# Kernel tuning notes

Hardware: AMD Instinct MI355X
Metric: run time of the kernel (lower is better)

The kernel has to match this reference:

```python
import jax, jax.numpy as jnp
import numpy as np

B, NR, NF, NH, NFH, D, HID = 32, 32, 128, 64, 64, 32, 256


def setup_inputs() -> dict:
    key = jax.random.key(0)
    ks = jax.random.split(key, 16)

    def w(k, o, i):
        return (jax.random.normal(k, (o, i), jnp.float32) / np.sqrt(i)).astype(jnp.float32)

    inp = {
        "robot": jax.random.normal(ks[0], (B, NR, D), jnp.float32),
        "frontier": jax.random.normal(ks[1], (B, NF, D), jnp.float32),
        "robot_history": jax.random.normal(ks[2], (B, NH, D), jnp.float32),
        "frontier_history": jax.random.normal(ks[3], (B, NFH, D), jnp.float32),
        "robot_frontier": jax.random.uniform(ks[4], (B, NR, NF), jnp.float32),
        "robot_past": jax.random.uniform(ks[5], (B, NR, NH), jnp.float32),
        "frontier_past": jax.random.uniform(ks[6], (B, NF, NFH), jnp.float32),
        # parameters (torch Linear convention: weight [out, in])
        "Wq": w(ks[7], D, D), "bq": jnp.zeros(D, jnp.float32),
        "Wk": w(ks[8], D, D), "bk": jnp.zeros(D, jnp.float32),
        "Wv": w(ks[9], D, D), "bv": jnp.zeros(D, jnp.float32),
        "Wn1": w(ks[10], HID, 2 * D), "bn1": jnp.zeros(HID, jnp.float32),
        "Wn2": w(ks[11], D, HID), "bn2": jnp.zeros(D, jnp.float32),
        "We1": w(ks[12], HID, 2 * D + 1), "be1": jnp.zeros(HID, jnp.float32),
        "We2": w(ks[13], 1, HID), "be2": jnp.zeros(1, jnp.float32),
    }
    return inp


def reference(robot, frontier, robot_history, frontier_history, robot_frontier,
              robot_past, frontier_past, Wq, bq, Wk, bk, Wv, bv,
              Wn1, bn1, Wn2, bn2, We1, be1, We2, be2):
    def lin(x, W, b):
        return x @ W.T + b

    def nmlp(h):
        return lin(jax.nn.relu(lin(h, Wn1, bn1)), Wn2, bn2)

    def emlp(h):
        return lin(jax.nn.relu(lin(h, We1, be1)), We2, be2)

    def intra(x):  # x: [b, n, D]
        q, k, v = lin(x, Wq, bq), lin(x, Wk, bk), lin(x, Wv, bv)
        e = jax.nn.softmax(jnp.einsum('bnd,bmd->bnm', q, k), axis=-1)
        agg = jnp.einsum('bnm,bmd->bnd', e, v)
        return x + nmlp(jnp.concatenate([x, agg], axis=-1))

    def inter(x, y, dis):  # x: [b,Nx,D], y: [b,Ny,D], dis: [b,Nx,Ny]
        xq, yk, yv = lin(x, Wq, bq), lin(y, Wk, bk), lin(y, Wv, bv)
        b, Nx, _ = x.shape
        Ny = y.shape[1]
        r_i = jnp.broadcast_to(xq[:, :, None, :], (b, Nx, Ny, D))
        f_j = jnp.broadcast_to(yk[:, None, :, :], (b, Nx, Ny, D))
        edge_input = jnp.concatenate([r_i, f_j, dis[..., None]], axis=-1)  # [b,Nx,Ny,65]
        score = emlp(edge_input)[..., 0]                                   # [b,Nx,Ny]
        e = jax.nn.softmax(score, axis=-1)
        agg = jnp.einsum('bnm,bmd->bnd', e, yv)
        x = x + nmlp(jnp.concatenate([x, agg], axis=-1))
        return e, x

    robot = intra(robot)
    frontier = intra(frontier)           # == per-sample intra on [1,Nf,D]
    robot_history = intra(robot_history)
    frontier_history = intra(frontier_history)
    _, robot = inter(robot, robot_history, robot_past)
    _, new_frontier = inter(frontier, frontier_history, frontier_past)
    edge, robot = inter(robot, new_frontier, robot_frontier)
    # original returns the intra-transformed frontier (split_frontier), not new_frontier
    return (robot, frontier, robot_history, frontier_history, edge)
```

## Files before the change

### kernel.cpp

```cpp
#include <hip/hip_runtime.h>

#define BATCH 32
#define NRr 32
#define NFf 128
#define NHh 64
#define NFHh 64
#define TI 4

__device__ __forceinline__ float dot4(float4 a, float4 b) {
    return fmaf(a.x, b.x, fmaf(a.y, b.y, fmaf(a.z, b.z, a.w * b.w)));
}

__global__ __launch_bounds__(256) void intra_kernel(
    const float* __restrict__ robot, const float* __restrict__ frontier,
    const float* __restrict__ rhist, const float* __restrict__ fhist,
    const float* __restrict__ Wq, const float* __restrict__ bq,
    const float* __restrict__ Wk, const float* __restrict__ bk,
    const float* __restrict__ Wv, const float* __restrict__ bv,
    const float* __restrict__ Wn1, const float* __restrict__ bn1,
    const float* __restrict__ Wn2, const float* __restrict__ bn2,
    float* __restrict__ o_robot, float* __restrict__ o_frontier,
    float* __restrict__ o_rh, float* __restrict__ o_fh)
{
    __shared__ __align__(16) float sXc[1024];
    __shared__ __align__(16) float sQ[1024];
    __shared__ __align__(16) float sQK[1024];
    __shared__ __align__(16) float sAgg[1024];
    __shared__ __align__(16) float sBig[8448];
    float* sS  = sBig;
    float* sXT = sBig + 4224;
    float* sT  = sBig;

    const int blk = blockIdx.x, tid = threadIdx.x;
    const float* xin; float* xout; int N, lgN, b, chunk;
    if (blk < 32)       { xin=robot;    xout=o_robot;    N=32;  lgN=5; b=blk;          chunk=0; }
    else if (blk < 160) { xin=frontier; xout=o_frontier; N=128; lgN=7; b=(blk-32)>>2;  chunk=(blk-32)&3; }
    else if (blk < 224) { xin=rhist;    xout=o_rh;       N=64;  lgN=6; b=(blk-160)>>1; chunk=(blk-160)&1; }
    else                { xin=fhist;    xout=o_fh;       N=64;  lgN=6; b=(blk-224)>>1; chunk=(blk-224)&1; }

    const int P = N + 4, P2 = N + 1;
    const float* xb = xin + (size_t)b * N * 32;
    const int r0 = chunk << 5;
    const int d = tid & 31;

    {
        int idx = tid;
        #pragma unroll
        for (int it = 0; it < 4; ++it, idx += 256)
            sXc[idx] = xb[(r0 << 5) + idx];
    }
    for (int idx = tid; idx < (N << 5); idx += 256) {
        int j = idx >> 5, d2 = idx & 31;
        sXT[d2 * P2 + j] = xb[idx];
    }
    __syncthreads();

    {
        const float4* wq4 = (const float4*)(Wq + (d << 5));
        float4 wq[8];
        #pragma unroll
        for (int k = 0; k < 8; ++k) wq[k] = wq4[k];
        const float bqd = bq[d];
        int idx = tid;
        #pragma unroll
        for (int it = 0; it < 4; ++it, idx += 256) {
            int r = idx >> 5;
            const float4* xr = (const float4*)(sXc + (r << 5));
            float a = bqd;
            #pragma unroll
            for (int k = 0; k < 8; ++k) a += dot4(wq[k], xr[k]);
            sQ[idx] = a;
        }
    }
    __syncthreads();

    {
        int idx = tid;
        #pragma unroll
        for (int it = 0; it < 4; ++it, idx += 256) {
            int r = idx >> 5, e = idx & 31;
            const float* qr = sQ + (r << 5);
            float a = 0.f;
            #pragma unroll
            for (int dd2 = 0; dd2 < 32; ++dd2)
                a = fmaf(Wk[dd2 * 32 + e], qr[dd2], a);
            sQK[idx] = a;
        }
    }
    __syncthreads();

    for (int idx = tid; idx < (N << 5); idx += 256) {
        int r = idx >> lgN, j = idx & (N - 1);
        const float* qr = sQK + (r << 5);
        float a = 0.f;
        #pragma unroll
        for (int e = 0; e < 32; ++e) a = fmaf(qr[e], sXT[e * P2 + j], a);
        sS[r * P + j] = a;
    }
    __syncthreads();

    {
        int r = tid >> 3, l = tid & 7;
        float* row = sS + r * P;
        float m = -1e30f;
        for (int j = l; j < N; j += 8) m = fmaxf(m, row[j]);
        m = fmaxf(m, __shfl_xor(m, 4));
        m = fmaxf(m, __shfl_xor(m, 2));
        m = fmaxf(m, __shfl_xor(m, 1));
        float s = 0.f;
        for (int j = l; j < N; j += 8) { float ev = __expf(row[j] - m); row[j] = ev; s += ev; }
        s += __shfl_xor(s, 4); s += __shfl_xor(s, 2); s += __shfl_xor(s, 1);
        float inv = 1.0f / s;
        for (int j = l; j < N; j += 8) row[j] *= inv;
    }
    __syncthreads();

    {
        int idx = tid;
        #pragma unroll
        for (int it = 0; it < 4; ++it, idx += 256) {
            int r = idx >> 5, d2 = idx & 31;
            const float* er = sS + r * P;
            const float* xtr = sXT + d2 * P2;
            float a = 0.f;
            for (int j = 0; j < N; ++j) a = fmaf(er[j], xtr[j], a);
            sQ[idx] = a;
        }
    }
    __syncthreads();

    {
        const float4* wv4 = (const float4*)(Wv + (d << 5));
        float4 wv[8];
        #pragma unroll
        for (int k = 0; k < 8; ++k) wv[k] = wv4[k];
        const float bvd = bv[d];
        int idx = tid;
        #pragma unroll
        for (int it = 0; it < 4; ++it, idx += 256) {
            int r = idx >> 5;
            const float4* zr = (const float4*)(sQ + (r << 5));
            float a = bvd;
            #pragma unroll
            for (int k = 0; k < 8; ++k) a += dot4(wv[k], zr[k]);
            sAgg[idx] = a;
        }
    }
    __syncthreads();

    {
        const float4* w14 = (const float4*)(Wn1 + (tid << 6));
        float4 w1r[16];
        #pragma unroll
        for (int k = 0; k < 16; ++k) w1r[k] = w14[k];
        const float b1 = bn1[tid];
        for (int r = 0; r < 32; ++r) {
            const float4* xr = (const float4*)(sXc + (r << 5));
            const float4* ar = (const float4*)(sAgg + (r << 5));
            float a = b1;
            #pragma unroll
            for (int k = 0; k < 8; ++k) a += dot4(w1r[k], xr[k]);
            #pragma unroll
            for (int k = 0; k < 8; ++k) a += dot4(w1r[8 + k], ar[k]);
            sT[(r << 8) + tid] = fmaxf(a, 0.f);
        }
    }
    __syncthreads();

    {
        const int rg = tid >> 5;
        float acc[4] = {0.f, 0.f, 0.f, 0.f};
        #pragma unroll
        for (int hc = 0; hc < 4; ++hc) {
            const float4* w24 = (const float4*)(Wn2 + (d << 8) + (hc << 6));
            float4 w2r[16];
            #pragma unroll
            for (int k = 0; k < 16; ++k) w2r[k] = w24[k];
            #pragma unroll
            for (int p = 0; p < 4; ++p) {
                int r = rg + (p << 3);
                const float4* tr = (const float4*)(sT + (r << 8) + (hc << 6));
                float a = 0.f;
                #pragma unroll
                for (int k = 0; k < 16; ++k) a += dot4(w2r[k], tr[k]);
                acc[p] += a;
            }
        }
        const float b2 = bn2[d];
        #pragma unroll
        for (int p = 0; p < 4; ++p) {
            int r = rg + (p << 3);
            xout[((size_t)b * N << 5) + ((r0 + r) << 5) + d] = sXc[(r << 5) + d] + b2 + acc[p];
        }
    }
}

__global__ __launch_bounds__(256) void pre_y_kernel(
    const float* __restrict__ yA, int NyA, float* __restrict__ wOutA, float* __restrict__ yvOutA, int nBlkA,
    const float* __restrict__ yB, int NyB, float* __restrict__ wOutB, float* __restrict__ yvOutB,
    int ghBase,
    const float* __restrict__ Wq, const float* __restrict__ bq,
    const float* __restrict__ Wk, const float* __restrict__ bk,
    const float* __restrict__ Wv, const float* __restrict__ bv,
    const float* __restrict__ We1, const float* __restrict__ be1,
    float* __restrict__ Gm, float* __restrict__ gvec,
    float* __restrict__ Hm, float* __restrict__ hbvec)
{
    __shared__ __align__(16) float sY[256], sK[256];
    const int blk = blockIdx.x, tid = threadIdx.x;

    if (blk >= ghBase) {
        const int hr = ((blk - ghBase) << 3) + (tid >> 5), e = tid & 31;
        const float* w1q = We1 + hr * 65;
        const float* w1k = w1q + 32;
        float aG = 0.f, aH = 0.f;
        #pragma unroll
        for (int d2 = 0; d2 < 32; ++d2) {
            aG = fmaf(w1q[d2], Wq[d2 * 32 + e], aG);
            aH = fmaf(w1k[d2], Wk[d2 * 32 + e], aH);
        }
        Gm[(hr << 5) + e] = aG;
        Hm[(hr << 5) + e] = aH;
        if (e == 0) {
            float ag = be1[hr], ahb = 0.f;
            #pragma unroll
            for (int d2 = 0; d2 < 32; ++d2) {
                ag  = fmaf(w1q[d2], bq[d2], ag);
                ahb = fmaf(w1k[d2], bk[d2], ahb);
            }
            gvec[hr] = ag;
            hbvec[hr] = ahb;
        }
        return;
    }

    const float* y; int Ny; float* wOut; float* yvOut; int idx;
    if (blk < nBlkA) { y=yA; Ny=NyA; wOut=wOutA; yvOut=yvOutA; idx=blk; }
    else             { y=yB; Ny=NyB; wOut=wOutB; yvOut=yvOutB; idx=blk-nBlkA; }
    const int chunks = Ny >> 3;
    const int b = idx / chunks, j0 = (idx - b * chunks) << 3;

    sY[tid] = y[((size_t)(b * Ny + j0)) * 32 + tid];
    __syncthreads();

    {
        int jl = tid >> 5, dd = tid & 31;
        const float4* wk4 = (const float4*)(Wk + (dd << 5));
        const float4* wv4 = (const float4*)(Wv + (dd << 5));
        const float4* yr = (const float4*)(sY + (jl << 5));
        float aK = bk[dd], aV = bv[dd];
        #pragma unroll
        for (int k = 0; k < 8; ++k) {
            float4 yv4 = yr[k];
            aK += dot4(wk4[k], yv4);
            aV += dot4(wv4[k], yv4);
        }
        sK[(jl << 5) + dd] = aK;
        yvOut[((size_t)(b * Ny + j0 + jl)) * 32 + dd] = aV;
    }
    __syncthreads();

    {
        const float* w1 = We1 + tid * 65 + 32;
        float acc[8] = {0,0,0,0,0,0,0,0};
        #pragma unroll
        for (int e = 0; e < 32; ++e) {
            float we = w1[e];
            #pragma unroll
            for (int jl = 0; jl < 8; ++jl)
                acc[jl] = fmaf(we, sK[(jl << 5) + e], acc[jl]);
        }
        float* wbase = wOut + (((size_t)b * 64 + (tid >> 2)) * Ny + j0) * 4 + (tid & 3);
        #pragma unroll
        for (int jl = 0; jl < 8; ++jl)
            wbase[jl << 2] = acc[jl];
    }
}

__global__ __launch_bounds__(256, 8) void inter_main_kernel(
    const float* __restrict__ xA, int NxA, const float* __restrict__ wA, const float* __restrict__ yvA,
    int NyA, const float* __restrict__ disA, float* __restrict__ outA, float* __restrict__ eA,
    float* __restrict__ wPreA, float* __restrict__ yvPreA, int nBlkA,
    const float* __restrict__ xB, int NxB, const float* __restrict__ wB, const float* __restrict__ yvB,
    int NyB, const float* __restrict__ disB, float* __restrict__ outB, float* __restrict__ eB,
    float* __restrict__ wPreB, float* __restrict__ yvPreB,
    const float* __restrict__ Gm, const float* __restrict__ gvec,
    const float* __restrict__ Hm, const float* __restrict__ hbvec,
    const float* __restrict__ Wv, const float* __restrict__ bv,
    const float* __restrict__ We1, const float* __restrict__ We2,
    const float* __restrict__ Wn1, const float* __restrict__ bn1,
    const float* __restrict__ Wn2, const float* __restrict__ bn2)
{
    __shared__ __align__(16) float sX[128];
    __shared__ __align__(16) float sQ[128];
    __shared__ __align__(16) float sAgg[128];
    __shared__ __align__(16) float sDis[512];
    __shared__ __align__(16) float sC[256];
    __shared__ __align__(16) float sW2[256];
    __shared__ __align__(16) float sS[512];
    __shared__ __align__(16) float sUT[1024];
    __shared__ __align__(16) float sPR[2048];

    const int blk = blockIdx.x, tid = threadIdx.x;
    const float* x; int Nx; const float* w; const float* yv; int Ny;
    const float* dis; float* outp; float* ep; float* wPre; float* yvPre; int idx;
    if (blk < nBlkA) { x=xA; Nx=NxA; w=wA; yv=yvA; Ny=NyA; dis=disA; outp=outA; ep=eA; wPre=wPreA; yvPre=yvPreA; idx=blk; }
    else             { x=xB; Nx=NxB; w=wB; yv=yvB; Ny=NyB; dis=disB; outp=outB; ep=eB; wPre=wPreB; yvPre=yvPreB; idx=blk-nBlkA; }
    const int lgNy = (Ny == 128) ? 7 : 6;
    const int tiles = Nx >> 2;
    const int b = idx / tiles, i0 = (idx - b * tiles) << 2;
    const float* xrow = x + ((size_t)(b * Nx + i0)) * 32;

    if (tid < 128) sX[tid] = xrow[tid];
    if (tid < Ny) {
        int il = tid >> (lgNy - 2), jq = tid & ((Ny >> 2) - 1);
        ((float4*)sDis)[(il << 5) + jq] =
            ((const float4*)(dis + ((size_t)(b * Nx + i0 + il)) * Ny))[jq];
    }
    __syncthreads();

    {
        const float* grow = Gm + (tid << 5);
        const float g0 = gvec[tid];
        float acc[TI];
        #pragma unroll
        for (int il = 0; il < TI; ++il) acc[il] = g0;
        #pragma unroll
        for (int e = 0; e < 32; ++e) {
            float we = grow[e];
            #pragma unroll
            for (int il = 0; il < TI; ++il)
                acc[il] = fmaf(we, sX[(il << 5) + e], acc[il]);
        }
        #pragma unroll
        for (int il = 0; il < TI; ++il) sUT[(il << 8) + tid] = acc[il];
        sC[tid] = We1[tid * 65 + 64];
        sW2[tid] = We2[tid];
    }
    __syncthreads();

    const int wv = tid >> 6, lane = tid & 63;
    {
        const int hc0 = wv << 4;
        const float4* wT4 = (const float4*)w + (size_t)(b * 64) * Ny;
        const float4* c4p = (const float4*)sC;
        const float4* p4p = (const float4*)sW2;
        if (Ny == 64) {
            float dv[TI];
            #pragma unroll
            for (int il = 0; il < TI; ++il) dv[il] = sDis[(il << 7) + lane];
            float acc[TI] = {0.f, 0.f, 0.f, 0.f};
            #pragma unroll
            for (int t = 0; t < 16; ++t) {
                int hc = hc0 + t;
                float4 w4 = wT4[((size_t)hc << 6) + lane];
                float4 c4 = c4p[hc], p4 = p4p[hc];
                #pragma unroll
                for (int il = 0; il < TI; ++il) {
                    float4 u4 = ((const float4*)(sUT + (il << 8)))[hc];
                    acc[il] = fmaf(p4.x, fmaxf(fmaf(c4.x, dv[il], u4.x + w4.x), 0.f), acc[il]);
                    acc[il] = fmaf(p4.y, fmaxf(fmaf(c4.y, dv[il], u4.y + w4.y), 0.f), acc[il]);
                    acc[il] = fmaf(p4.z, fmaxf(fmaf(c4.z, dv[il], u4.z + w4.z), 0.f), acc[il]);
                    acc[il] = fmaf(p4.w, fmaxf(fmaf(c4.w, dv[il], u4.w + w4.w), 0.f), acc[il]);
                }
            }
            #pragma unroll
            for (int il = 0; il < TI; ++il)
                sPR[(wv << 9) + (il << 7) + lane] = acc[il];
        } else {
            float dv0[TI], dv1[TI];
            #pragma unroll
            for (int il = 0; il < TI; ++il) {
                dv0[il] = sDis[(il << 7) + lane];
                dv1[il] = sDis[(il << 7) + 64 + lane];
            }
            float acc0[TI] = {0.f, 0.f, 0.f, 0.f};
            float acc1[TI] = {0.f, 0.f, 0.f, 0.f};
            #pragma unroll
            for (int t = 0; t < 16; ++t) {
                int hc = hc0 + t;
                float4 wa = wT4[((size_t)hc << 7) + lane];
                float4 wb = wT4[((size_t)hc << 7) + 64 + lane];
                float4 c4 = c4p[hc], p4 = p4p[hc];
                #pragma unroll
                for (int il = 0; il < TI; ++il) {
                    float4 u4 = ((const float4*)(sUT + (il << 8)))[hc];
                    acc0[il] = fmaf(p4.x, fmaxf(fmaf(c4.x, dv0[il], u4.x + wa.x), 0.f), acc0[il]);
                    acc0[il] = fmaf(p4.y, fmaxf(fmaf(c4.y, dv0[il], u4.y + wa.y), 0.f), acc0[il]);
                    acc0[il] = fmaf(p4.z, fmaxf(fmaf(c4.z, dv0[il], u4.z + wa.z), 0.f), acc0[il]);
                    acc0[il] = fmaf(p4.w, fmaxf(fmaf(c4.w, dv0[il], u4.w + wa.w), 0.f), acc0[il]);
                    acc1[il] = fmaf(p4.x, fmaxf(fmaf(c4.x, dv1[il], u4.x + wb.x), 0.f), acc1[il]);
                    acc1[il] = fmaf(p4.y, fmaxf(fmaf(c4.y, dv1[il], u4.y + wb.y), 0.f), acc1[il]);
                    acc1[il] = fmaf(p4.z, fmaxf(fmaf(c4.z, dv1[il], u4.z + wb.z), 0.f), acc1[il]);
                    acc1[il] = fmaf(p4.w, fmaxf(fmaf(c4.w, dv1[il], u4.w + wb.w), 0.f), acc1[il]);
                }
            }
            #pragma unroll
            for (int il = 0; il < TI; ++il) {
                sPR[(wv << 9) + (il << 7) + lane] = acc0[il];
                sPR[(wv << 9) + (il << 7) + 64 + lane] = acc1[il];
            }
        }
    }
    __syncthreads();

    {
        const int base = (wv << 7) + lane;
        float v0 = sPR[base] + sPR[512 + base] + sPR[1024 + base] + sPR[1536 + base];
        float v1 = -1e30f;
        if (Ny == 128) {
            const int b2 = base + 64;
            v1 = sPR[b2] + sPR[512 + b2] + sPR[1024 + b2] + sPR[1536 + b2];
        }
        float m = fmaxf(v0, v1);
        #pragma unroll
        for (int msk = 32; msk; msk >>= 1) m = fmaxf(m, __shfl_xor(m, msk));
        float e0 = __expf(v0 - m);
        float e1 = (Ny == 128) ? __expf(v1 - m) : 0.f;
        float s = e0 + e1;
        #pragma unroll
        for (int msk = 32; msk; msk >>= 1) s += __shfl_xor(s, msk);
        float inv = 1.0f / s;
        e0 *= inv; e1 *= inv;
        sS[base] = e0;
        if (Ny == 128) sS[base + 64] = e1;
        if (ep) {
            float* erow = ep + ((size_t)(b * Nx + i0 + wv)) * Ny;
            erow[lane] = e0;
            if (Ny == 128) erow[64 + lane] = e1;
        }
    }

    {
        const int dd = lane & 31, jg = lane >> 5;
        const float* yvg = yv + ((size_t)(b * Ny) << 5);
        float p = 0.f;
        #pragma unroll 8
        for (int j = jg; j < Ny; j += 2)
            p = fmaf(sS[(wv << 7) + j], yvg[(j << 5) + dd], p);
        p += __shfl_xor(p, 32);
        if (jg == 0) sAgg[(wv << 5) + dd] = p;
    }
    __syncthreads();

    {
        const float4* w14 = (const float4*)(Wn1 + (tid << 6));
        const float b1 = bn1[tid];
        float acc[TI];
        #pragma unroll
        for (int il = 0; il < TI; ++il) acc[il] = b1;
        #pragma unroll
        for (int k = 0; k < 8; ++k) {
            float4 wa = w14[k];
            #pragma unroll
            for (int il = 0; il < TI; ++il)
                acc[il] += dot4(wa, ((const float4*)(sX + (il << 5)))[k]);
        }
        #pragma unroll
        for (int k = 0; k < 8; ++k) {
            float4 wb = w14[8 + k];
            #pragma unroll
            for (int il = 0; il < TI; ++il)
                acc[il] += dot4(wb, ((const float4*)(sAgg + (il << 5)))[k]);
        }
        __syncthreads();
        #pragma unroll
        for (int il = 0; il < TI; ++il) sUT[(il << 8) + tid] = fmaxf(acc[il], 0.f);
    }
    __syncthreads();

    {
        const int hg = tid >> 5, dd = tid & 31;
        const float4* w24 = (const float4*)(Wn2 + (dd << 8) + (hg << 5));
        float4 w2r[8];
        #pragma unroll
        for (int k = 0; k < 8; ++k) w2r[k] = w24[k];
        float p[TI] = {0.f, 0.f, 0.f, 0.f};
        #pragma unroll
        for (int k = 0; k < 8; ++k) {
            #pragma unroll
            for (int il = 0; il < TI; ++il)
                p[il] += dot4(w2r[k], ((const float4*)(sUT + (il << 8) + (hg << 5)))[k]);
        }
        #pragma unroll
        for (int il = 0; il < TI; ++il) sPR[(hg << 7) + (il << 5) + dd] = p[il];
    }
    __syncthreads();
    if (tid < 128) {
        int il = tid >> 5, dd = tid & 31;
        float a = bn2[dd] + sX[tid];
        #pragma unroll
        for (int hg = 0; hg < 8; ++hg) a += sPR[(hg << 7) + tid];
        outp[((size_t)(b * Nx + i0 + il)) * 32 + dd] = a;
        if (wPre) sQ[tid] = a;
    }

    if (wPre) {
        __syncthreads();
        if (tid < 128) {
            int il = tid >> 5, dd = tid & 31;
            const float4* wm4 = (const float4*)(Wv + (dd << 5));
            const float4* orow = (const float4*)(sQ + (il << 5));
            float a = bv[dd];
            #pragma unroll
            for (int k = 0; k < 8; ++k) a += dot4(wm4[k], orow[k]);
            yvPre[(((size_t)(b * Nx + i0 + il)) << 5) + dd] = a;
        }
        {
            const float* hrow = Hm + (tid << 5);
            const float hb0 = hbvec[tid];
            float acc[4];
            #pragma unroll
            for (int il = 0; il < 4; ++il) acc[il] = hb0;
            #pragma unroll
            for (int e = 0; e < 32; ++e) {
                float we = hrow[e];
                #pragma unroll
                for (int il = 0; il < 4; ++il)
                    acc[il] = fmaf(we, sQ[(il << 5) + e], acc[il]);
            }
            float* wbase = wPre + (((size_t)b * 64 + (tid >> 2)) * Nx + i0) * 4 + (tid & 3);
            #pragma unroll
            for (int il = 0; il < 4; ++il)
                wbase[il << 2] = acc[il];
        }
    }
}

extern "C" void kernel_launch(void* const* d_in, const int* in_sizes, int n_in,
                              void* d_out, int out_size, void* d_ws, size_t ws_size,
                              hipStream_t stream) {
    const float* robot          = (const float*)d_in[0];
    const float* frontier       = (const float*)d_in[1];
    const float* rh             = (const float*)d_in[2];
    const float* fh             = (const float*)d_in[3];
    const float* robot_frontier = (const float*)d_in[4];
    const float* robot_past     = (const float*)d_in[5];
    const float* frontier_past  = (const float*)d_in[6];
    const float* Wq  = (const float*)d_in[7];  const float* bq  = (const float*)d_in[8];
    const float* Wk  = (const float*)d_in[9];  const float* bk  = (const float*)d_in[10];
    const float* Wv  = (const float*)d_in[11]; const float* bv  = (const float*)d_in[12];
    const float* Wn1 = (const float*)d_in[13]; const float* bn1 = (const float*)d_in[14];
    const float* Wn2 = (const float*)d_in[15]; const float* bn2 = (const float*)d_in[16];
    const float* We1 = (const float*)d_in[17]; const float* be1 = (const float*)d_in[18];
    const float* We2 = (const float*)d_in[19];

    float* out = (float*)d_out;
    float* out_robot    = out;
    float* out_frontier = out + 32768;
    float* out_rh       = out + 163840;
    float* out_fh       = out + 229376;
    float* out_edge     = out + 294912;

    float* W = (float*)d_ws;
    float* robot1 = W;
    float* robot2 = W + 32768;
    float* nf     = W + 65536;
    float* w5     = W + 196608;
    float* yv5    = W + 720896;
    float* w6     = W + 786432;
    float* yv6    = W + 1310720;
    float* w7     = W + 1376256;
    float* yv7    = W + 2424832;
    float* Gm     = W + 2555904;
    float* gvec   = W + 2564096;
    float* Hm     = W + 2564352;
    float* hbvec  = W + 2572544;

    intra_kernel<<<288, 256, 0, stream>>>(robot, frontier, rh, fh,
        Wq, bq, Wk, bk, Wv, bv, Wn1, bn1, Wn2, bn2,
        robot1, out_frontier, out_rh, out_fh);

    pre_y_kernel<<<544, 256, 0, stream>>>(
        out_rh, NHh, w5, yv5, BATCH * NHh / 8,
        out_fh, NFHh, w6, yv6,
        512,
        Wq, bq, Wk, bk, Wv, bv, We1, be1,
        Gm, gvec, Hm, hbvec);

    inter_main_kernel<<<1280, 256, 0, stream>>>(
        robot1, NRr, w5, yv5, NHh, robot_past, robot2,
        (float*)nullptr, (float*)nullptr, (float*)nullptr, BATCH * (NRr / TI),
        out_frontier, NFf, w6, yv6, NFHh, frontier_past, nf,
        (float*)nullptr, w7, yv7,
        Gm, gvec, Hm, hbvec, Wv, bv, We1, We2, Wn1, bn1, Wn2, bn2);

    inter_main_kernel<<<256, 256, 0, stream>>>(
        robot2, NRr, w7, yv7, NFf, robot_frontier, out_robot, out_edge,
        (float*)nullptr, (float*)nullptr, BATCH * (NRr / TI),
        robot2, NRr, w7, yv7, NFf, robot_frontier, out_robot, out_edge,
        (float*)nullptr, (float*)nullptr,
        Gm, gvec, Hm, hbvec, Wv, bv, We1, We2, Wn1, bn1, Wn2, bn2);
}
```

Measured before the change: 198.4 us.

## Split intra kernel into 8-row chunks to quadruple block count

Each intra_kernel block now processes 8 query rows instead of 32, so the grid grows from 288 to 1152 blocks and each thread handles one output element per stage. Shared memory per block shrinks and launch bounds request 4 blocks per CU to raise occupancy. The cost is redundant work: every block still loads and transposes the full N-row input, and the Wn1/Wn2 weights are re-read by four times as many blocks.

```diff
diff --git a/kernel.cpp b/kernel.cpp
--- a/kernel.cpp
+++ b/kernel.cpp
@@ -11,7 +11,7 @@
     return fmaf(a.x, b.x, fmaf(a.y, b.y, fmaf(a.z, b.z, a.w * b.w)));
 }
 
-__global__ __launch_bounds__(256) void intra_kernel(
+__global__ __launch_bounds__(256, 4) void intra_kernel(
     const float* __restrict__ robot, const float* __restrict__ frontier,
     const float* __restrict__ rhist, const float* __restrict__ fhist,
     const float* __restrict__ Wq, const float* __restrict__ bq,
@@ -22,33 +22,29 @@
     float* __restrict__ o_robot, float* __restrict__ o_frontier,
     float* __restrict__ o_rh, float* __restrict__ o_fh)
 {
-    __shared__ __align__(16) float sXc[1024];
-    __shared__ __align__(16) float sQ[1024];
-    __shared__ __align__(16) float sQK[1024];
-    __shared__ __align__(16) float sAgg[1024];
-    __shared__ __align__(16) float sBig[8448];
+    __shared__ __align__(16) float sXc[256];
+    __shared__ __align__(16) float sQ[256];
+    __shared__ __align__(16) float sQK[256];
+    __shared__ __align__(16) float sAgg[256];
+    __shared__ __align__(16) float sBig[5184];
     float* sS  = sBig;
-    float* sXT = sBig + 4224;
+    float* sXT = sBig + 1056;
     float* sT  = sBig;
 
     const int blk = blockIdx.x, tid = threadIdx.x;
     const float* xin; float* xout; int N, lgN, b, chunk;
-    if (blk < 32)       { xin=robot;    xout=o_robot;    N=32;  lgN=5; b=blk;          chunk=0; }
-    else if (blk < 160) { xin=frontier; xout=o_frontier; N=128; lgN=7; b=(blk-32)>>2;  chunk=(blk-32)&3; }
-    else if (blk < 224) { xin=rhist;    xout=o_rh;       N=64;  lgN=6; b=(blk-160)>>1; chunk=(blk-160)&1; }
-    else                { xin=fhist;    xout=o_fh;       N=64;  lgN=6; b=(blk-224)>>1; chunk=(blk-224)&1; }
+    if (blk < 128)      { xin=robot;    xout=o_robot;    N=32;  lgN=5; b=blk>>2;            chunk=blk&3; }
+    else if (blk < 640) { xin=frontier; xout=o_frontier; N=128; lgN=7; b=(blk-128)>>4;      chunk=(blk-128)&15; }
+    else if (blk < 896) { xin=rhist;    xout=o_rh;       N=64;  lgN=6; b=(blk-640)>>3;      chunk=(blk-640)&7; }
+    else                { xin=fhist;    xout=o_fh;       N=64;  lgN=6; b=(blk-896)>>3;      chunk=(blk-896)&7; }
 
     const int P = N + 4, P2 = N + 1;
     const float* xb = xin + (size_t)b * N * 32;
-    const int r0 = chunk << 5;
+    const int r0 = chunk << 3;
     const int d = tid & 31;
-
-    {
-        int idx = tid;
-        #pragma unroll
-        for (int it = 0; it < 4; ++it, idx += 256)
-            sXc[idx] = xb[(r0 << 5) + idx];
-    }
+    const int rloc = tid >> 5;
+
+    sXc[tid] = xb[(r0 << 5) + tid];
     for (int idx = tid; idx < (N << 5); idx += 256) {
         int j = idx >> 5, d2 = idx & 31;
         sXT[d2 * P2 + j] = xb[idx];
@@ -57,39 +53,25 @@
 
     {
         const float4* wq4 = (const float4*)(Wq + (d << 5));
-        float4 wq[8];
-        #pragma unroll
-        for (int k = 0; k < 8; ++k) wq[k] = wq4[k];
-        const float bqd = bq[d];
-        int idx = tid;
-        #pragma unroll
-        for (int it = 0; it < 4; ++it, idx += 256) {
-            int r = idx >> 5;
-            const float4* xr = (const float4*)(sXc + (r << 5));
-            float a = bqd;
-            #pragma unroll
-            for (int k = 0; k < 8; ++k) a += dot4(wq[k], xr[k]);
-            sQ[idx] = a;
-        }
-    }
-    __syncthreads();
-
-    {
-        int idx = tid;
-        #pragma unroll
-        for (int it = 0; it < 4; ++it, idx += 256) {
-            int r = idx >> 5, e = idx & 31;
-            const float* qr = sQ + (r << 5);
-            float a = 0.f;
-            #pragma unroll
-            for (int dd2 = 0; dd2 < 32; ++dd2)
-                a = fmaf(Wk[dd2 * 32 + e], qr[dd2], a);
-            sQK[idx] = a;
-        }
-    }
-    __syncthreads();
-
-    for (int idx = tid; idx < (N << 5); idx += 256) {
+        const float4* xr = (const float4*)(sXc + (rloc << 5));
+        float a = bq[d];
+        #pragma unroll
+        for (int k = 0; k < 8; ++k) a += dot4(wq4[k], xr[k]);
+        sQ[tid] = a;
+    }
+    __syncthreads();
+
+    {
+        const float* qr = sQ + (rloc << 5);
+        float a = 0.f;
+        #pragma unroll
+        for (int dd2 = 0; dd2 < 32; ++dd2)
+            a = fmaf(Wk[dd2 * 32 + d], qr[dd2], a);
+        sQK[tid] = a;
+    }
+    __syncthreads();
+
+    for (int idx = tid; idx < (8 << lgN); idx += 256) {
         int r = idx >> lgN, j = idx & (N - 1);
         const float* qr = sQK + (r << 5);
         float a = 0.f;
@@ -100,51 +82,36 @@
     __syncthreads();
 
     {
-        int r = tid >> 3, l = tid & 7;
-        float* row = sS + r * P;
+        float* row = sS + rloc * P;
         float m = -1e30f;
-        for (int j = l; j < N; j += 8) m = fmaxf(m, row[j]);
-        m = fmaxf(m, __shfl_xor(m, 4));
-        m = fmaxf(m, __shfl_xor(m, 2));
-        m = fmaxf(m, __shfl_xor(m, 1));
+        for (int j = d; j < N; j += 32) m = fmaxf(m, row[j]);
+        #pragma unroll
+        for (int msk = 16; msk; msk >>= 1) m = fmaxf(m, __shfl_xor(m, msk));
         float s = 0.f;
-        for (int j = l; j < N; j += 8) { float ev = __expf(row[j] - m); row[j] = ev; s += ev; }
-        s += __shfl_xor(s, 4); s += __shfl_xor(s, 2); s += __shfl_xor(s, 1);
+        for (int j = d; j < N; j += 32) { float ev = __expf(row[j] - m); row[j] = ev; s += ev; }
+        #pragma unroll
+        for (int msk = 16; msk; msk >>= 1) s += __shfl_xor(s, msk);
         float inv = 1.0f / s;
-        for (int j = l; j < N; j += 8) row[j] *= inv;
-    }
-    __syncthreads();
-
-    {
-        int idx = tid;
-        #pragma unroll
-        for (int it = 0; it < 4; ++it, idx += 256) {
-            int r = idx >> 5, d2 = idx & 31;
-            const float* er = sS + r * P;
-            const float* xtr = sXT + d2 * P2;
-            float a = 0.f;
-            for (int j = 0; j < N; ++j) a = fmaf(er[j], xtr[j], a);
-            sQ[idx] = a;
-        }
+        for (int j = d; j < N; j += 32) row[j] *= inv;
+    }
+    __syncthreads();
+
+    {
+        const float* er = sS + rloc * P;
+        const float* xtr = sXT + d * P2;
+        float a = 0.f;
+        for (int j = 0; j < N; ++j) a = fmaf(er[j], xtr[j], a);
+        sQ[tid] = a;
     }
     __syncthreads();
 
     {
         const float4* wv4 = (const float4*)(Wv + (d << 5));
-        float4 wv[8];
-        #pragma unroll
-        for (int k = 0; k < 8; ++k) wv[k] = wv4[k];
-        const float bvd = bv[d];
-        int idx = tid;
-        #pragma unroll
-        for (int it = 0; it < 4; ++it, idx += 256) {
-            int r = idx >> 5;
-            const float4* zr = (const float4*)(sQ + (r << 5));
-            float a = bvd;
-            #pragma unroll
-            for (int k = 0; k < 8; ++k) a += dot4(wv[k], zr[k]);
-            sAgg[idx] = a;
-        }
+        const float4* zr = (const float4*)(sQ + (rloc << 5));
+        float a = bv[d];
+        #pragma unroll
+        for (int k = 0; k < 8; ++k) a += dot4(wv4[k], zr[k]);
+        sAgg[tid] = a;
     }
     __syncthreads();
 
@@ -154,7 +121,8 @@
         #pragma unroll
         for (int k = 0; k < 16; ++k) w1r[k] = w14[k];
         const float b1 = bn1[tid];
-        for (int r = 0; r < 32; ++r) {
+        #pragma unroll
+        for (int r = 0; r < 8; ++r) {
             const float4* xr = (const float4*)(sXc + (r << 5));
             const float4* ar = (const float4*)(sAgg + (r << 5));
             float a = b1;
@@ -168,30 +136,12 @@
     __syncthreads();
 
     {
-        const int rg = tid >> 5;
-        float acc[4] = {0.f, 0.f, 0.f, 0.f};
-        #pragma unroll
-        for (int hc = 0; hc < 4; ++hc) {
-            const float4* w24 = (const float4*)(Wn2 + (d << 8) + (hc << 6));
-            float4 w2r[16];
-            #pragma unroll
-            for (int k = 0; k < 16; ++k) w2r[k] = w24[k];
-            #pragma unroll
-            for (int p = 0; p < 4; ++p) {
-                int r = rg + (p << 3);
-                const float4* tr = (const float4*)(sT + (r << 8) + (hc << 6));
-                float a = 0.f;
-                #pragma unroll
-                for (int k = 0; k < 16; ++k) a += dot4(w2r[k], tr[k]);
-                acc[p] += a;
-            }
-        }
-        const float b2 = bn2[d];
-        #pragma unroll
-        for (int p = 0; p < 4; ++p) {
-            int r = rg + (p << 3);
-            xout[((size_t)b * N << 5) + ((r0 + r) << 5) + d] = sXc[(r << 5) + d] + b2 + acc[p];
-        }
+        const float4* w24 = (const float4*)(Wn2 + (d << 8));
+        const float4* tr = (const float4*)(sT + (rloc << 8));
+        float a = 0.f;
+        #pragma unroll 8
+        for (int k = 0; k < 64; ++k) a += dot4(w24[k], tr[k]);
+        xout[((size_t)b * N << 5) + ((r0 + rloc) << 5) + d] = sXc[tid] + bn2[d] + a;
     }
 }
 
@@ -567,7 +517,7 @@
     float* Hm     = W + 2564352;
     float* hbvec  = W + 2572544;
 
-    intra_kernel<<<288, 256, 0, stream>>>(robot, frontier, rh, fh,
+    intra_kernel<<<1152, 256, 0, stream>>>(robot, frontier, rh, fh,
         Wq, bq, Wk, bk, Wv, bv, Wn1, bn1, Wn2, bn2,
         robot1, out_frontier, out_rh, out_fh);
 
```

Result: slower. 225.1 us (+13.5%).
